# Kernel tuning notes

Hardware: AMD Instinct MI355X
Metric: run time of the kernel (lower is better)

## Reference

```python
import jax, jax.numpy as jnp
import numpy as np

N = 262144
E = N * 32
C_W = 7.0 / np.pi  # Wendland C2 2D normalization


def kernel_gradient(q, dirs, h):
    # torchSPHv2 wendland gradient: -dir * C/h^3 * 20 q (1-q)^3, q = r/h in [0,1]
    mag = (C_W / h ** 3) * 20.0 * q * (1.0 - q) ** 3
    return -dirs * mag[:, None]


def setup_inputs() -> dict:
    key = jax.random.key(0)
    ks = jax.random.split(key, 10)
    pos = lambda k: jax.random.uniform(k, (N,), dtype=jnp.float32) + 0.5  # keep strictly positive
    fluidArea = pos(ks[0]) * 1e-3
    fluidActualArea = pos(ks[1]) * 1e-3
    fluidRestDensity = pos(ks[2]) * 1000.0
    fluidDensity = pos(ks[3])
    fluidPressure2 = jax.random.uniform(ks[4], (N,), dtype=jnp.float32) * 1e3
    fluidPredictedVelocity = jax.random.normal(ks[5], (N, 2), dtype=jnp.float32)
    fluidPredAccel = jax.random.normal(ks[6], (N, 2), dtype=jnp.float32)
    fluidNeighbors = jax.random.randint(ks[7], (2, E), 0, N, dtype=jnp.int32)
    fluidRadialDistances = jax.random.uniform(ks[8], (E,), dtype=jnp.float32)
    d = jax.random.normal(ks[9], (E, 2), dtype=jnp.float32)
    fluidDistances = d / (jnp.linalg.norm(d, axis=1, keepdims=True) + 1e-7)
    return {
        'fluidArea': fluidArea, 'fluidActualArea': fluidActualArea,
        'fluidRestDensity': fluidRestDensity, 'fluidDensity': fluidDensity,
        'fluidPressure2': fluidPressure2,
        'fluidPredictedVelocity': fluidPredictedVelocity,
        'fluidPredAccel': fluidPredAccel,
        'fluidRadialDistances': fluidRadialDistances,
        'fluidDistances': fluidDistances,
        'fluidNeighbors': fluidNeighbors,
        'support': 0.05, 'dt': 0.002,
    }


def reference(fluidArea, fluidActualArea, fluidRestDensity, fluidDensity,
              fluidPressure2, fluidPredictedVelocity, fluidPredAccel,
              fluidRadialDistances, fluidDistances, fluidNeighbors,
              support, dt):
    seg = lambda v, i: jax.ops.segment_sum(v, i, num_segments=N)
    i = fluidNeighbors[0]
    j = fluidNeighbors[1]
    grad = kernel_gradient(fluidRadialDistances, fluidDistances, support)  # [E,2]
    grad2 = jnp.einsum('nd,nd->n', grad, grad)

    # --- alpha (fluid term + final) ---
    kSum1 = seg(fluidActualArea[j][:, None] * grad, i)                       # [N,2]
    kSum2 = seg((fluidActualArea ** 2 / (fluidArea * fluidRestDensity))[j] * grad2, i)
    fac = -dt ** 2 * fluidActualArea
    mass = fluidArea * fluidRestDensity
    alpha = fac / mass * jnp.einsum('nd,nd->n', kSum1, kSum1) + fac * kSum2

    # --- fluid pressure acceleration ---
    facA = -(fluidArea * fluidRestDensity)[j]
    p = fluidPressure2 / (fluidDensity * fluidRestDensity) ** 2
    fluidAccelTerm = seg((facA * (p[i] + p[j]))[:, None] * grad, i)          # [N,2]

    # --- source term (velocity divergence) ---
    facS = -dt * fluidActualArea[j]
    vij = fluidPredictedVelocity[i] - fluidPredictedVelocity[j]
    source = seg(facS * jnp.einsum('nd,nd->n', vij, grad), i)                # [N]

    # --- updated pressure fluid kernel sum ---
    facP = dt ** 2 * fluidActualArea[j]
    aij = fluidPredAccel[i] - fluidPredAccel[j]
    kernelSum = seg(jnp.einsum('nd,nd->n', facP[:, None] * aij, grad), i)    # [N]

    return jnp.concatenate([alpha[:, None], fluidAccelTerm,
                            source[:, None], kernelSum[:, None]], axis=1)  # [N,5]
```

## Files before the change

kernel.cpp:

```cpp
#include <hip/hip_runtime.h>
#include <math.h>


#define PB        512
#define PB_SHIFT  9
#define SLICES    8
#define CSTRIDE   16
#define NR        8
#define BIN_EDGES 2048
#define TILE      1024

typedef float v2f __attribute__((ext_vector_type(2)));

__device__ __forceinline__ void ldsbar() {
    asm volatile("s_waitcnt lgkmcnt(0)" ::: "memory");
    __builtin_amdgcn_s_barrier();
    asm volatile("" ::: "memory");
}

static inline size_t align256(size_t x) { return (x + 255) & ~(size_t)255; }

__global__ __launch_bounds__(256) void pre_kernel(
    const float*  __restrict__ area,
    const float*  __restrict__ actualArea,
    const float*  __restrict__ restDensity,
    const float*  __restrict__ density,
    const float*  __restrict__ pressure2,
    const float2* __restrict__ vel,
    const float2* __restrict__ accel,
    float4* __restrict__ pre2,
    int*    __restrict__ cursor, int ncursor,
    float*  __restrict__ accz, int nacc,
    int n) {
    int t = blockIdx.x * blockDim.x + threadIdx.x;
    int stride = gridDim.x * blockDim.x;
    for (int k = t; k < ncursor; k += stride) cursor[k] = 0;
    for (int k = t; k < nacc; k += stride) accz[k] = 0.f;
    if (t >= n) return;
    float m  = area[t] * restDensity[t];
    float dr = density[t] * restDensity[t];
    float p  = pressure2[t] / (dr * dr);
    float aa = actualArea[t];
    float2 v  = vel[t];
    float2 ac = accel[t];
    pre2[2 * (size_t)t]     = make_float4(p, m / aa, aa, aa * aa / m);
    pre2[2 * (size_t)t + 1] = make_float4(v.x, v.y, ac.x, ac.y);
}

__global__ __launch_bounds__(256) void bin_kernel(
    const int*    __restrict__ nbr,
    const float*  __restrict__ rad,
    const float2* __restrict__ dirs,
    const float*  __restrict__ supp,
    int*          __restrict__ cursor,
    unsigned int* __restrict__ pay32,
    int cap, int nb, int estart, int eend, int E) {
    __shared__ float s3[BIN_EDGES * 3];
    __shared__ int   sD[BIN_EDGES];
    __shared__ int lcount[512];
    __shared__ int lclaim[512];
    __shared__ int lstart[512];
    int tid = threadIdx.x;
    int x   = blockIdx.x & (NR - 1);
    for (int k = tid; k < 512; k += 256) lcount[k] = 0;
    ldsbar();
    int e0 = estart + blockIdx.x * BIN_EDGES + tid;

    int jj[8]; float qq[8]; v2f dd[8]; int pk[8];
#pragma unroll
    for (int k = 0; k < 8; ++k) {
        int e = e0 + k * 256;
        pk[k] = -1; jj[k] = 0; qq[k] = 0.f; dd[k] = (v2f){0.f, 0.f};
        if (e < eend) {
            jj[k] = __builtin_nontemporal_load(nbr + E + e);
            qq[k] = __builtin_nontemporal_load(rad + e);
            dd[k] = __builtin_nontemporal_load((const v2f*)dirs + e);
            int i = __builtin_nontemporal_load(nbr + e);
            int b = i >> PB_SHIFT;
            int r = atomicAdd(&lcount[b], 1);
            pk[k] = (b << 21) | ((i & (PB - 1)) << 12) | r;
        }
    }
    ldsbar();
    if (tid >= 64) {
        for (int k = tid - 64; k < nb; k += 192) {
            int c = lcount[k];
            lclaim[k] = c ? atomicAdd(&cursor[(size_t)(k * NR + x) * CSTRIDE], c) : 0;
        }
    } else {
        int running = 0;
        for (int c = 0; c < 8; ++c) {
            int orig = lcount[c * 64 + tid];
            int v = orig;
#pragma unroll
            for (int off = 1; off < 64; off <<= 1) {
                int u = __shfl_up(v, off, 64);
                if (tid >= off) v += u;
            }
            lstart[c * 64 + tid] = running + v - orig;
            running += __shfl(v, 63, 64);
        }
    }
    ldsbar();

    float h  = supp[0];
    float kc = 20.0f * (7.0f / 3.14159265358979323846f) / (h * h * h);
    int cap3  = cap * 3;
    int cap24 = cap * 3 * NR;

#pragma unroll
    for (int k = 0; k < 8; ++k) {
        if (pk[k] < 0) continue;
        int b  = pk[k] >> 21;
        int li = (pk[k] >> 12) & (PB - 1);
        int r  = pk[k] & 2047;
        float  q = qq[k];
        v2f    d = dd[k];
        float om  = 1.0f - q;
        float mag = kc * q * om * om * om;
        float gx = -d.x * mag;
        float gy = -d.y * mag;
        int slot = lstart[b] + r;
        s3[slot * 3 + 0] = __int_as_float((jj[k] << PB_SHIFT) | li);
        s3[slot * 3 + 1] = gx;
        s3[slot * 3 + 2] = gy;
        int g = lclaim[b] + r;
        sD[slot] = (g < cap) ? (b * cap24 + x * cap3 + g * 3) : -1;
    }
    ldsbar();
    int total3 = (lstart[511] + lcount[511]) * 3;
    for (int dwi = tid; dwi < total3; dwi += 256) {
        int rec = dwi / 3;
        int f   = dwi - rec * 3;
        int gd  = sD[rec];
        if (gd >= 0) pay32[gd + f] = __float_as_uint(s3[dwi]);
    }
}

__global__ __launch_bounds__(256) void reduce_kernel(
    const unsigned int* __restrict__ pay32,
    const int*    __restrict__ cursor, int cap,
    const float4* __restrict__ pre2,
    const float*  __restrict__ dtp,
    float*        __restrict__ partials,
    int accum, int n) {
    __shared__ float s7[7][TILE];
    __shared__ int   lhist[PB];
    __shared__ int   lofs[PB];
    __shared__ float ptab[PB];
    int b   = blockIdx.x >> 3;
    int s   = blockIdx.x & (NR - 1);
    int tid = threadIdx.x;

    int p0 = (b << PB_SHIFT) + tid;
    int p1 = p0 + 256;
    float pi0 = (p0 < n) ? pre2[2 * (size_t)p0].x : 0.f;
    float pi1 = (p1 < n) ? pre2[2 * (size_t)p1].x : 0.f;
    ptab[tid] = pi0; ptab[tid + 256] = pi1;
    float a0[7] = {0.f, 0.f, 0.f, 0.f, 0.f, 0.f, 0.f};
    float a1[7] = {0.f, 0.f, 0.f, 0.f, 0.f, 0.f, 0.f};
    float dt  = dtp[0];
    float dt2 = dt * dt;

    int cnt = cursor[(size_t)(b * NR + s) * CSTRIDE];
    if (cnt > cap) cnt = cap;
    size_t RB = (size_t)(b * NR + s) * cap * 3;
    int r0 = tid * 4;

    float4 c0v, c1v, c2v, n0v, n1v, n2v;
    if (cnt > 0) {
        int rb = r0;
        int rc_ = (rb + 4 <= cap) ? rb : (cap - 4);
        const float4* g = (const float4*)(pay32 + RB + (size_t)rc_ * 3);
        c0v = g[0]; c1v = g[1]; c2v = g[2];
    }
    for (int T = 0; T < cnt; T += TILE) {
        lhist[tid] = 0; lhist[tid + 256] = 0;
        if (T + TILE < cnt) {
            int rb = T + TILE + r0;
            int rc_ = (rb + 4 <= cap) ? rb : (cap - 4);
            const float4* g = (const float4*)(pay32 + RB + (size_t)rc_ * 3);
            n0v = g[0]; n1v = g[1]; n2v = g[2];
        }
        int rb = T + r0;
        bool v0 = rb < cnt, v1 = rb + 1 < cnt, v2 = rb + 2 < cnt, v3 = rb + 3 < cnt;
        int jli0 = __float_as_int(c0v.x); float gx0 = c0v.y, gy0 = c0v.z;
        int jli1 = __float_as_int(c0v.w); float gx1 = c1v.x, gy1 = c1v.y;
        int jli2 = __float_as_int(c1v.z); float gx2 = c1v.w, gy2 = c2v.x;
        int jli3 = __float_as_int(c2v.y); float gx3 = c2v.z, gy3 = c2v.w;
        int li0 = jli0 & (PB - 1), li1 = jli1 & (PB - 1);
        int li2 = jli2 & (PB - 1), li3 = jli3 & (PB - 1);
        size_t j0 = v0 ? (size_t)(jli0 >> PB_SHIFT) : 0;
        size_t j1 = v1 ? (size_t)(jli1 >> PB_SHIFT) : 0;
        size_t j2 = v2 ? (size_t)(jli2 >> PB_SHIFT) : 0;
        size_t j3 = v3 ? (size_t)(jli3 >> PB_SHIFT) : 0;
        float4 ja0 = pre2[2 * j0], jb0 = pre2[2 * j0 + 1];
        float4 ja1 = pre2[2 * j1], jb1 = pre2[2 * j1 + 1];
        float4 ja2 = pre2[2 * j2], jb2 = pre2[2 * j2 + 1];
        float4 ja3 = pre2[2 * j3], jb3 = pre2[2 * j3 + 1];
        ldsbar();
        if (v0) atomicAdd(&lhist[li0], 1);
        if (v1) atomicAdd(&lhist[li1], 1);
        if (v2) atomicAdd(&lhist[li2], 1);
        if (v3) atomicAdd(&lhist[li3], 1);
        ldsbar();
        if (tid < 64) {
            int running = 0;
            for (int c = 0; c < 8; ++c) {
                int orig = lhist[c * 64 + tid];
                int v = orig;
#pragma unroll
                for (int off = 1; off < 64; off <<= 1) {
                    int u = __shfl_up(v, off, 64);
                    if (tid >= off) v += u;
                }
                lofs[c * 64 + tid] = running + v - orig;
                running += __shfl(v, 63, 64);
            }
        }
        ldsbar();
#define SCAT(vv, li, jaa, jbb, gxx, gyy)                                     \
        if (vv) {                                                            \
            int sl = atomicAdd(&lofs[li], 1);                                \
            float C0 = jaa.z * gxx;                                          \
            float C1 = jaa.z * gyy;                                          \
            float C2 = jaa.w * (gxx * gxx + gyy * gyy);                      \
            float rc = -(ptab[li] + jaa.x) * jaa.y;                          \
            s7[0][sl] = C0;      s7[1][sl] = C1;      s7[2][sl] = C2;        \
            s7[3][sl] = rc * C0; s7[4][sl] = rc * C1;                        \
            s7[5][sl] = dt  * (jbb.x * C0 + jbb.y * C1);                     \
            s7[6][sl] = dt2 * (jbb.z * C0 + jbb.w * C1);                     \
        }
        SCAT(v0, li0, ja0, jb0, gx0, gy0)
        SCAT(v1, li1, ja1, jb1, gx1, gy1)
        SCAT(v2, li2, ja2, jb2, gx2, gy2)
        SCAT(v3, li3, ja3, jb3, gx3, gy3)
#undef SCAT
        ldsbar();
        {
            int e0 = lofs[tid], h0 = lhist[tid];
            for (int r = e0 - h0; r < e0; ++r) {
                a0[0] += s7[0][r]; a0[1] += s7[1][r]; a0[2] += s7[2][r];
                a0[3] += s7[3][r]; a0[4] += s7[4][r];
                a0[5] += s7[5][r]; a0[6] += s7[6][r];
            }
            int e1 = lofs[tid + 256], h1 = lhist[tid + 256];
            for (int r = e1 - h1; r < e1; ++r) {
                a1[0] += s7[0][r]; a1[1] += s7[1][r]; a1[2] += s7[2][r];
                a1[3] += s7[3][r]; a1[4] += s7[4][r];
                a1[5] += s7[5][r]; a1[6] += s7[6][r];
            }
        }
        ldsbar();
        c0v = n0v; c1v = n1v; c2v = n2v;
    }

    float* dst = partials + ((size_t)b * SLICES + s) * (PB * 7);
    {
        float4 va = (p0 < n) ? pre2[2 * (size_t)p0 + 1]
                             : make_float4(0.f, 0.f, 0.f, 0.f);
        float src = a0[5] - dt  * (va.x * a0[0] + va.y * a0[1]);
        float ker = dt2 * (va.z * a0[0] + va.w * a0[1]) - a0[6];
        float* d = dst + (size_t)tid * 7;
        if (accum) {
            d[0] += a0[0]; d[1] += a0[1]; d[2] += a0[2]; d[3] += a0[3];
            d[4] += a0[4]; d[5] += src;   d[6] += ker;
        } else {
            d[0] = a0[0]; d[1] = a0[1]; d[2] = a0[2]; d[3] = a0[3];
            d[4] = a0[4]; d[5] = src;   d[6] = ker;
        }
    }
    {
        float4 va = (p1 < n) ? pre2[2 * (size_t)p1 + 1]
                             : make_float4(0.f, 0.f, 0.f, 0.f);
        float src = a1[5] - dt  * (va.x * a1[0] + va.y * a1[1]);
        float ker = dt2 * (va.z * a1[0] + va.w * a1[1]) - a1[6];
        float* d = dst + (size_t)(tid + 256) * 7;
        if (accum) {
            d[0] += a1[0]; d[1] += a1[1]; d[2] += a1[2]; d[3] += a1[3];
            d[4] += a1[4]; d[5] += src;   d[6] += ker;
        } else {
            d[0] = a1[0]; d[1] = a1[1]; d[2] = a1[2]; d[3] = a1[3];
            d[4] = a1[4]; d[5] = src;   d[6] = ker;
        }
    }
}

__global__ void edge_kernel(const int* __restrict__ nbr,
                            const float* __restrict__ rad,
                            const float2* __restrict__ dirs,
                            const float4* __restrict__ pre2,
                            const float* __restrict__ supp,
                            const float* __restrict__ dtp,
                            float* __restrict__ acc, int E) {
    int e = blockIdx.x * blockDim.x + threadIdx.x;
    if (e >= E) return;
    float h = supp[0], dt = dtp[0];
    float kc = 20.0f * (7.0f / 3.14159265358979323846f) / (h * h * h);
    int i = nbr[e];
    int j = nbr[E + e];
    float  q = rad[e];
    float2 d = dirs[e];
    float om  = 1.0f - q;
    float mag = kc * q * om * om * om;
    float gx = -d.x * mag;
    float gy = -d.y * mag;
    float g2 = gx * gx + gy * gy;
    float4 ja = pre2[2 * (size_t)j];
    float4 jb = pre2[2 * (size_t)j + 1];
    float4 ia = pre2[2 * (size_t)i];
    float4 ib = pre2[2 * (size_t)i + 1];
    float aaj = ja.z;
    float m   = ja.y * aaj;
    float pp  = -m * (ia.x + ja.x);
    float vdotg = (ib.x - jb.x) * gx + (ib.y - jb.y) * gy;
    float adotg = (ib.z - jb.z) * gx + (ib.w - jb.w) * gy;
    float* base = acc + (size_t)i * 8;
    atomicAdd(base + 0, aaj * gx);
    atomicAdd(base + 1, aaj * gy);
    atomicAdd(base + 2, ja.w * g2);
    atomicAdd(base + 3, pp * gx);
    atomicAdd(base + 4, pp * gy);
    atomicAdd(base + 5, -dt * aaj * vdotg);
    atomicAdd(base + 6, dt * dt * aaj * adotg);
}

__global__ __launch_bounds__(256) void fin_kernel(
    const float* __restrict__ area,
    const float* __restrict__ actualArea,
    const float* __restrict__ restDensity,
    const float* __restrict__ dtp,
    const float* __restrict__ data, int mode, int nslice,
    float* __restrict__ out, int n) {
    int t = blockIdx.x * blockDim.x + threadIdx.x;
    if (t >= n) return;
    float s0 = 0, s1 = 0, s2 = 0, s3 = 0, s4 = 0, s5 = 0, s6 = 0;
    if (mode == 0) {
        const float* base = data + ((size_t)(t >> PB_SHIFT) * SLICES) * (PB * 7)
                                 + (size_t)(t & (PB - 1)) * 7;
        for (int s = 0; s < nslice; ++s) {
            const float* p = base + (size_t)s * (PB * 7);
            s0 += p[0]; s1 += p[1]; s2 += p[2]; s3 += p[3];
            s4 += p[4]; s5 += p[5]; s6 += p[6];
        }
    } else {
        const float* a = data + (size_t)t * 8;
        s0 = a[0]; s1 = a[1]; s2 = a[2]; s3 = a[3];
        s4 = a[4]; s5 = a[5]; s6 = a[6];
    }
    float dt   = dtp[0];
    float fac  = -dt * dt * actualArea[t];
    float mass = area[t] * restDensity[t];
    float alpha = fac / mass * (s0 * s0 + s1 * s1) + fac * s2;
    float* o = out + (size_t)t * 5;
    o[0] = alpha;
    o[1] = s3;
    o[2] = s4;
    o[3] = s5;
    o[4] = s6;
}

extern "C" void kernel_launch(void* const* d_in, const int* in_sizes, int n_in,
                              void* d_out, int out_size, void* d_ws, size_t ws_size,
                              hipStream_t stream) {
    const float* area        = (const float*)d_in[0];
    const float* actualArea  = (const float*)d_in[1];
    const float* restDensity = (const float*)d_in[2];
    const float* density     = (const float*)d_in[3];
    const float* pressure2   = (const float*)d_in[4];
    const float2* vel        = (const float2*)d_in[5];
    const float2* accel      = (const float2*)d_in[6];
    const float* rad         = (const float*)d_in[7];
    const float2* dirs       = (const float2*)d_in[8];
    const int*   nbr         = (const int*)d_in[9];
    const float* supp        = (const float*)d_in[10];
    const float* dtp         = (const float*)d_in[11];
    float* out = (float*)d_out;

    int N = in_sizes[0];
    int E = in_sizes[7];
    int nb = (N + PB - 1) >> PB_SHIFT;

    size_t sz_cur   = (size_t)nb * NR * CSTRIDE * 8 * sizeof(int);
    size_t off_pre  = align256(sz_cur);
    size_t sz_pre   = (size_t)N * 8 * sizeof(float);
    size_t off_part = align256(off_pre + sz_pre);
    size_t sz_part  = (size_t)nb * SLICES * PB * 7 * sizeof(float);
    size_t off_pay  = align256(off_part + sz_part);

    int* cursor     = (int*)d_ws;
    float4* pre2    = (float4*)((char*)d_ws + off_pre);
    float* partials = (float*)((char*)d_ws + off_part);

    int nchunk = 0, cap = 0;
    if (nb <= 512 && ws_size > off_pay) {
        for (int c = 1; c <= 8; c *= 2) {
            long long Ec = (E + c - 1) / c;
            double mean = (double)Ec / ((double)nb * NR);
            long long need = (long long)(mean + 8.0 * sqrt(mean) + 64.0);
            need = (need + 63) & ~63ll;
            if (off_pay + (size_t)nb * NR * need * 12 <= ws_size) {
                nchunk = c; cap = (int)need; break;
            }
        }
    }

    int bs = 256;
    int grid_n = (N + bs - 1) / bs;
    if (nchunk > 0) {
        unsigned int* pay32 = (unsigned int*)((char*)d_ws + off_pay);
        int ncursor = nb * NR * CSTRIDE * nchunk;
        pre_kernel<<<grid_n, bs, 0, stream>>>(
            area, actualArea, restDensity, density, pressure2, vel, accel,
            pre2, cursor, ncursor, (float*)nullptr, 0, N);
        int Ec  = (E + nchunk - 1) / nchunk;
        for (int c = 0; c < nchunk; ++c) {
            int es = c * Ec;
            int ee = es + Ec; if (ee > E) ee = E;
            if (es >= ee) break;
            int* curC = cursor + (size_t)c * nb * NR * CSTRIDE;
            int nblk = (ee - es + BIN_EDGES - 1) / BIN_EDGES;
            bin_kernel<<<nblk, bs, 0, stream>>>(
                nbr, rad, dirs, supp, curC, pay32, cap, nb, es, ee, E);
            reduce_kernel<<<nb * NR, bs, 0, stream>>>(
                pay32, curC, cap, pre2, dtp, partials, (c > 0) ? 1 : 0, N);
        }
        fin_kernel<<<grid_n, bs, 0, stream>>>(
            area, actualArea, restDensity, dtp, partials, 0, SLICES, out, N);
    } else {
        float* acc = partials;
        pre_kernel<<<grid_n, bs, 0, stream>>>(
            area, actualArea, restDensity, density, pressure2, vel, accel,
            pre2, cursor, 0, acc, N * 8, N);
        edge_kernel<<<(E + bs - 1) / bs, bs, 0, stream>>>(
            nbr, rad, dirs, pre2, supp, dtp, acc, E);
        fin_kernel<<<grid_n, bs, 0, stream>>>(
            area, actualArea, restDensity, dtp, acc, 1, 0, out, N);
    }
}
```

Measured before the change: 397.9 us.

## Halve reduce partial slices, pack bin records as float4, vectorize partial I/O

Each reduce block now processes two of the eight bin slices for a particle block, so there are four partial slices instead of eight and less partial traffic for the final kernel. Partials are padded to eight floats and written and read as two 16-byte vectors with nontemporal hints. The bin kernel stores each record together with its destination in a single float4 in LDS and writes it out as one 12-byte store instead of three scalar stores. The dt scaling and the pressure-coefficient product move out of the per-edge scatter into the per-particle accumulation, which trims LDS traffic per edge. In exchange the reduce grid is half as large, which lowers parallelism and may leave the GPU less well occupied.

Result: faster. 389.4 us (-2.1%).

```diff
diff --git a/kernel.cpp b/kernel.cpp
--- a/kernel.cpp
+++ b/kernel.cpp
@@ -4,13 +4,14 @@
 
 #define PB        512
 #define PB_SHIFT  9
-#define SLICES    8
+#define NR        8
+#define NSLICE    4
 #define CSTRIDE   16
-#define NR        8
 #define BIN_EDGES 2048
 #define TILE      1024
 
 typedef float v2f __attribute__((ext_vector_type(2)));
+typedef float v4f __attribute__((ext_vector_type(4)));
 
 __device__ __forceinline__ void ldsbar() {
     asm volatile("s_waitcnt lgkmcnt(0)" ::: "memory");
@@ -55,8 +56,7 @@
     int*          __restrict__ cursor,
     unsigned int* __restrict__ pay32,
     int cap, int nb, int estart, int eend, int E) {
-    __shared__ float s3[BIN_EDGES * 3];
-    __shared__ int   sD[BIN_EDGES];
+    __shared__ float4 srec[BIN_EDGES];
     __shared__ int lcount[512];
     __shared__ int lclaim[512];
     __shared__ int lstart[512];
@@ -120,20 +120,21 @@
         float mag = kc * q * om * om * om;
         float gx = -d.x * mag;
         float gy = -d.y * mag;
-        int slot = lstart[b] + r;
-        s3[slot * 3 + 0] = __int_as_float((jj[k] << PB_SHIFT) | li);
-        s3[slot * 3 + 1] = gx;
-        s3[slot * 3 + 2] = gy;
-        int g = lclaim[b] + r;
-        sD[slot] = (g < cap) ? (b * cap24 + x * cap3 + g * 3) : -1;
+        int g  = lclaim[b] + r;
+        int gd = (g < cap) ? (b * cap24 + x * cap3 + g * 3) : -1;
+        srec[lstart[b] + r] = make_float4(
+            __int_as_float((jj[k] << PB_SHIFT) | li), gx, gy, __int_as_float(gd));
     }
     ldsbar();
-    int total3 = (lstart[511] + lcount[511]) * 3;
-    for (int dwi = tid; dwi < total3; dwi += 256) {
-        int rec = dwi / 3;
-        int f   = dwi - rec * 3;
-        int gd  = sD[rec];
-        if (gd >= 0) pay32[gd + f] = __float_as_uint(s3[dwi]);
+    int total = lstart[511] + lcount[511];
+    for (int r = tid; r < total; r += 256) {
+        float4 rec = srec[r];
+        int gd = __float_as_int(rec.w);
+        if (gd >= 0) {
+            uint3 w = make_uint3(__float_as_uint(rec.x), __float_as_uint(rec.y),
+                                 __float_as_uint(rec.z));
+            *(uint3*)(pay32 + gd) = w;
+        }
     }
 }
 
@@ -144,12 +145,12 @@
     const float*  __restrict__ dtp,
     float*        __restrict__ partials,
     int accum, int n) {
-    __shared__ float s7[7][TILE];
+    __shared__ float s7[6][TILE];
     __shared__ int   lhist[PB];
     __shared__ int   lofs[PB];
     __shared__ float ptab[PB];
-    int b   = blockIdx.x >> 3;
-    int s   = blockIdx.x & (NR - 1);
+    int b   = blockIdx.x >> 2;
+    int sb  = blockIdx.x & (NSLICE - 1);
     int tid = threadIdx.x;
 
     int p0 = (b << PB_SHIFT) + tid;
@@ -159,129 +160,142 @@
     ptab[tid] = pi0; ptab[tid + 256] = pi1;
     float a0[7] = {0.f, 0.f, 0.f, 0.f, 0.f, 0.f, 0.f};
     float a1[7] = {0.f, 0.f, 0.f, 0.f, 0.f, 0.f, 0.f};
+
+    int r0 = tid * 4;
+    for (int rg = 0; rg < 2; ++rg) {
+        int s = sb + rg * NSLICE;
+        int cnt = cursor[(size_t)(b * NR + s) * CSTRIDE];
+        if (cnt > cap) cnt = cap;
+        size_t RB = (size_t)(b * NR + s) * cap * 3;
+
+        v4f c0v, c1v, c2v, n0v, n1v, n2v;
+        if (cnt > 0) {
+            int rb = r0;
+            int rc_ = (rb + 4 <= cap) ? rb : (cap - 4);
+            const v4f* g = (const v4f*)(pay32 + RB + (size_t)rc_ * 3);
+            c0v = __builtin_nontemporal_load(g);
+            c1v = __builtin_nontemporal_load(g + 1);
+            c2v = __builtin_nontemporal_load(g + 2);
+        }
+        for (int T = 0; T < cnt; T += TILE) {
+            lhist[tid] = 0; lhist[tid + 256] = 0;
+            if (T + TILE < cnt) {
+                int rb = T + TILE + r0;
+                int rc_ = (rb + 4 <= cap) ? rb : (cap - 4);
+                const v4f* g = (const v4f*)(pay32 + RB + (size_t)rc_ * 3);
+                n0v = __builtin_nontemporal_load(g);
+                n1v = __builtin_nontemporal_load(g + 1);
+                n2v = __builtin_nontemporal_load(g + 2);
+            }
+            int rb = T + r0;
+            bool v0 = rb < cnt, v1 = rb + 1 < cnt, v2 = rb + 2 < cnt, v3 = rb + 3 < cnt;
+            int jli0 = __float_as_int(c0v.x); float gx0 = c0v.y, gy0 = c0v.z;
+            int jli1 = __float_as_int(c0v.w); float gx1 = c1v.x, gy1 = c1v.y;
+            int jli2 = __float_as_int(c1v.z); float gx2 = c1v.w, gy2 = c2v.x;
+            int jli3 = __float_as_int(c2v.y); float gx3 = c2v.z, gy3 = c2v.w;
+            int li0 = jli0 & (PB - 1), li1 = jli1 & (PB - 1);
+            int li2 = jli2 & (PB - 1), li3 = jli3 & (PB - 1);
+            size_t j0 = v0 ? (size_t)(jli0 >> PB_SHIFT) : 0;
+            size_t j1 = v1 ? (size_t)(jli1 >> PB_SHIFT) : 0;
+            size_t j2 = v2 ? (size_t)(jli2 >> PB_SHIFT) : 0;
+            size_t j3 = v3 ? (size_t)(jli3 >> PB_SHIFT) : 0;
+            float4 ja0 = pre2[2 * j0], jb0 = pre2[2 * j0 + 1];
+            float4 ja1 = pre2[2 * j1], jb1 = pre2[2 * j1 + 1];
+            float4 ja2 = pre2[2 * j2], jb2 = pre2[2 * j2 + 1];
+            float4 ja3 = pre2[2 * j3], jb3 = pre2[2 * j3 + 1];
+            ldsbar();
+            if (v0) atomicAdd(&lhist[li0], 1);
+            if (v1) atomicAdd(&lhist[li1], 1);
+            if (v2) atomicAdd(&lhist[li2], 1);
+            if (v3) atomicAdd(&lhist[li3], 1);
+            ldsbar();
+            if (tid < 64) {
+                int running = 0;
+                for (int c = 0; c < 8; ++c) {
+                    int orig = lhist[c * 64 + tid];
+                    int v = orig;
+#pragma unroll
+                    for (int off = 1; off < 64; off <<= 1) {
+                        int u = __shfl_up(v, off, 64);
+                        if (tid >= off) v += u;
+                    }
+                    lofs[c * 64 + tid] = running + v - orig;
+                    running += __shfl(v, 63, 64);
+                }
+            }
+            ldsbar();
+#define SCAT(vv, li, jaa, jbb, gxx, gyy)                                     \
+            if (vv) {                                                        \
+                int sl = atomicAdd(&lofs[li], 1);                            \
+                float C0 = jaa.z * gxx;                                      \
+                float C1 = jaa.z * gyy;                                      \
+                s7[0][sl] = C0;                                              \
+                s7[1][sl] = C1;                                              \
+                s7[2][sl] = jaa.w * (gxx * gxx + gyy * gyy);                 \
+                s7[3][sl] = -(ptab[li] + jaa.x) * jaa.y;                     \
+                s7[4][sl] = jbb.x * C0 + jbb.y * C1;                         \
+                s7[5][sl] = jbb.z * C0 + jbb.w * C1;                         \
+            }
+            SCAT(v0, li0, ja0, jb0, gx0, gy0)
+            SCAT(v1, li1, ja1, jb1, gx1, gy1)
+            SCAT(v2, li2, ja2, jb2, gx2, gy2)
+            SCAT(v3, li3, ja3, jb3, gx3, gy3)
+#undef SCAT
+            ldsbar();
+            {
+                int e0 = lofs[tid], h0 = lhist[tid];
+                for (int r = e0 - h0; r < e0; ++r) {
+                    float C0 = s7[0][r], C1 = s7[1][r], rc = s7[3][r];
+                    a0[0] += C0; a0[1] += C1; a0[2] += s7[2][r];
+                    a0[3] += rc * C0; a0[4] += rc * C1;
+                    a0[5] += s7[4][r]; a0[6] += s7[5][r];
+                }
+                int e1 = lofs[tid + 256], h1 = lhist[tid + 256];
+                for (int r = e1 - h1; r < e1; ++r) {
+                    float C0 = s7[0][r], C1 = s7[1][r], rc = s7[3][r];
+                    a1[0] += C0; a1[1] += C1; a1[2] += s7[2][r];
+                    a1[3] += rc * C0; a1[4] += rc * C1;
+                    a1[5] += s7[4][r]; a1[6] += s7[5][r];
+                }
+            }
+            ldsbar();
+            c0v = n0v; c1v = n1v; c2v = n2v;
+        }
+    }
+
     float dt  = dtp[0];
     float dt2 = dt * dt;
-
-    int cnt = cursor[(size_t)(b * NR + s) * CSTRIDE];
-    if (cnt > cap) cnt = cap;
-    size_t RB = (size_t)(b * NR + s) * cap * 3;
-    int r0 = tid * 4;
-
-    float4 c0v, c1v, c2v, n0v, n1v, n2v;
-    if (cnt > 0) {
-        int rb = r0;
-        int rc_ = (rb + 4 <= cap) ? rb : (cap - 4);
-        const float4* g = (const float4*)(pay32 + RB + (size_t)rc_ * 3);
-        c0v = g[0]; c1v = g[1]; c2v = g[2];
-    }
-    for (int T = 0; T < cnt; T += TILE) {
-        lhist[tid] = 0; lhist[tid + 256] = 0;
-        if (T + TILE < cnt) {
-            int rb = T + TILE + r0;
-            int rc_ = (rb + 4 <= cap) ? rb : (cap - 4);
-            const float4* g = (const float4*)(pay32 + RB + (size_t)rc_ * 3);
-            n0v = g[0]; n1v = g[1]; n2v = g[2];
-        }
-        int rb = T + r0;
-        bool v0 = rb < cnt, v1 = rb + 1 < cnt, v2 = rb + 2 < cnt, v3 = rb + 3 < cnt;
-        int jli0 = __float_as_int(c0v.x); float gx0 = c0v.y, gy0 = c0v.z;
-        int jli1 = __float_as_int(c0v.w); float gx1 = c1v.x, gy1 = c1v.y;
-        int jli2 = __float_as_int(c1v.z); float gx2 = c1v.w, gy2 = c2v.x;
-        int jli3 = __float_as_int(c2v.y); float gx3 = c2v.z, gy3 = c2v.w;
-        int li0 = jli0 & (PB - 1), li1 = jli1 & (PB - 1);
-        int li2 = jli2 & (PB - 1), li3 = jli3 & (PB - 1);
-        size_t j0 = v0 ? (size_t)(jli0 >> PB_SHIFT) : 0;
-        size_t j1 = v1 ? (size_t)(jli1 >> PB_SHIFT) : 0;
-        size_t j2 = v2 ? (size_t)(jli2 >> PB_SHIFT) : 0;
-        size_t j3 = v3 ? (size_t)(jli3 >> PB_SHIFT) : 0;
-        float4 ja0 = pre2[2 * j0], jb0 = pre2[2 * j0 + 1];
-        float4 ja1 = pre2[2 * j1], jb1 = pre2[2 * j1 + 1];
-        float4 ja2 = pre2[2 * j2], jb2 = pre2[2 * j2 + 1];
-        float4 ja3 = pre2[2 * j3], jb3 = pre2[2 * j3 + 1];
-        ldsbar();
-        if (v0) atomicAdd(&lhist[li0], 1);
-        if (v1) atomicAdd(&lhist[li1], 1);
-        if (v2) atomicAdd(&lhist[li2], 1);
-        if (v3) atomicAdd(&lhist[li3], 1);
-        ldsbar();
-        if (tid < 64) {
-            int running = 0;
-            for (int c = 0; c < 8; ++c) {
-                int orig = lhist[c * 64 + tid];
-                int v = orig;
-#pragma unroll
-                for (int off = 1; off < 64; off <<= 1) {
-                    int u = __shfl_up(v, off, 64);
-                    if (tid >= off) v += u;
-                }
-                lofs[c * 64 + tid] = running + v - orig;
-                running += __shfl(v, 63, 64);
-            }
-        }
-        ldsbar();
-#define SCAT(vv, li, jaa, jbb, gxx, gyy)                                     \
-        if (vv) {                                                            \
-            int sl = atomicAdd(&lofs[li], 1);                                \
-            float C0 = jaa.z * gxx;                                          \
-            float C1 = jaa.z * gyy;                                          \
-            float C2 = jaa.w * (gxx * gxx + gyy * gyy);                      \
-            float rc = -(ptab[li] + jaa.x) * jaa.y;                          \
-            s7[0][sl] = C0;      s7[1][sl] = C1;      s7[2][sl] = C2;        \
-            s7[3][sl] = rc * C0; s7[4][sl] = rc * C1;                        \
-            s7[5][sl] = dt  * (jbb.x * C0 + jbb.y * C1);                     \
-            s7[6][sl] = dt2 * (jbb.z * C0 + jbb.w * C1);                     \
-        }
-        SCAT(v0, li0, ja0, jb0, gx0, gy0)
-        SCAT(v1, li1, ja1, jb1, gx1, gy1)
-        SCAT(v2, li2, ja2, jb2, gx2, gy2)
-        SCAT(v3, li3, ja3, jb3, gx3, gy3)
-#undef SCAT
-        ldsbar();
-        {
-            int e0 = lofs[tid], h0 = lhist[tid];
-            for (int r = e0 - h0; r < e0; ++r) {
-                a0[0] += s7[0][r]; a0[1] += s7[1][r]; a0[2] += s7[2][r];
-                a0[3] += s7[3][r]; a0[4] += s7[4][r];
-                a0[5] += s7[5][r]; a0[6] += s7[6][r];
-            }
-            int e1 = lofs[tid + 256], h1 = lhist[tid + 256];
-            for (int r = e1 - h1; r < e1; ++r) {
-                a1[0] += s7[0][r]; a1[1] += s7[1][r]; a1[2] += s7[2][r];
-                a1[3] += s7[3][r]; a1[4] += s7[4][r];
-                a1[5] += s7[5][r]; a1[6] += s7[6][r];
-            }
-        }
-        ldsbar();
-        c0v = n0v; c1v = n1v; c2v = n2v;
-    }
-
-    float* dst = partials + ((size_t)b * SLICES + s) * (PB * 7);
+    v4f* dst = (v4f*)(partials + ((size_t)b * NSLICE + sb) * (PB * 8));
     {
         float4 va = (p0 < n) ? pre2[2 * (size_t)p0 + 1]
                              : make_float4(0.f, 0.f, 0.f, 0.f);
-        float src = a0[5] - dt  * (va.x * a0[0] + va.y * a0[1]);
-        float ker = dt2 * (va.z * a0[0] + va.w * a0[1]) - a0[6];
-        float* d = dst + (size_t)tid * 7;
+        float src = dt  * (a0[5] - (va.x * a0[0] + va.y * a0[1]));
+        float ker = dt2 * ((va.z * a0[0] + va.w * a0[1]) - a0[6]);
+        v4f w0 = {a0[0], a0[1], a0[2], a0[3]};
+        v4f w1 = {a0[4], src, ker, 0.f};
+        v4f* d = dst + (size_t)tid * 2;
         if (accum) {
-            d[0] += a0[0]; d[1] += a0[1]; d[2] += a0[2]; d[3] += a0[3];
-            d[4] += a0[4]; d[5] += src;   d[6] += ker;
+            v4f o0 = d[0], o1 = d[1];
+            d[0] = w0 + o0; d[1] = w1 + o1;
         } else {
-            d[0] = a0[0]; d[1] = a0[1]; d[2] = a0[2]; d[3] = a0[3];
-            d[4] = a0[4]; d[5] = src;   d[6] = ker;
+            __builtin_nontemporal_store(w0, d);
+            __builtin_nontemporal_store(w1, d + 1);
         }
     }
     {
         float4 va = (p1 < n) ? pre2[2 * (size_t)p1 + 1]
                              : make_float4(0.f, 0.f, 0.f, 0.f);
-        float src = a1[5] - dt  * (va.x * a1[0] + va.y * a1[1]);
-        float ker = dt2 * (va.z * a1[0] + va.w * a1[1]) - a1[6];
-        float* d = dst + (size_t)(tid + 256) * 7;
+        float src = dt  * (a1[5] - (va.x * a1[0] + va.y * a1[1]));
+        float ker = dt2 * ((va.z * a1[0] + va.w * a1[1]) - a1[6]);
+        v4f w0 = {a1[0], a1[1], a1[2], a1[3]};
+        v4f w1 = {a1[4], src, ker, 0.f};
+        v4f* d = dst + (size_t)(tid + 256) * 2;
         if (accum) {
-            d[0] += a1[0]; d[1] += a1[1]; d[2] += a1[2]; d[3] += a1[3];
-            d[4] += a1[4]; d[5] += src;   d[6] += ker;
+            v4f o0 = d[0], o1 = d[1];
+            d[0] = w0 + o0; d[1] = w1 + o1;
         } else {
-            d[0] = a1[0]; d[1] = a1[1]; d[2] = a1[2]; d[3] = a1[3];
-            d[4] = a1[4]; d[5] = src;   d[6] = ker;
+            __builtin_nontemporal_store(w0, d);
+            __builtin_nontemporal_store(w1, d + 1);
         }
     }
 }
@@ -336,12 +350,14 @@
     if (t >= n) return;
     float s0 = 0, s1 = 0, s2 = 0, s3 = 0, s4 = 0, s5 = 0, s6 = 0;
     if (mode == 0) {
-        const float* base = data + ((size_t)(t >> PB_SHIFT) * SLICES) * (PB * 7)
-                                 + (size_t)(t & (PB - 1)) * 7;
+        const v4f* base = (const v4f*)data
+            + ((size_t)(t >> PB_SHIFT) * NSLICE) * (PB * 2)
+            + (size_t)(t & (PB - 1)) * 2;
         for (int s = 0; s < nslice; ++s) {
-            const float* p = base + (size_t)s * (PB * 7);
-            s0 += p[0]; s1 += p[1]; s2 += p[2]; s3 += p[3];
-            s4 += p[4]; s5 += p[5]; s6 += p[6];
+            v4f q0 = __builtin_nontemporal_load(base + (size_t)s * (PB * 2));
+            v4f q1 = __builtin_nontemporal_load(base + (size_t)s * (PB * 2) + 1);
+            s0 += q0.x; s1 += q0.y; s2 += q0.z; s3 += q0.w;
+            s4 += q1.x; s5 += q1.y; s6 += q1.z;
         }
     } else {
         const float* a = data + (size_t)t * 8;
@@ -385,7 +401,9 @@
     size_t off_pre  = align256(sz_cur);
     size_t sz_pre   = (size_t)N * 8 * sizeof(float);
     size_t off_part = align256(off_pre + sz_pre);
-    size_t sz_part  = (size_t)nb * SLICES * PB * 7 * sizeof(float);
+    size_t sz_partA = (size_t)nb * NSLICE * PB * 8 * sizeof(float);
+    size_t sz_partB = (size_t)N * 8 * sizeof(float);
+    size_t sz_part  = sz_partA > sz_partB ? sz_partA : sz_partB;
     size_t off_pay  = align256(off_part + sz_part);
 
     int* cursor     = (int*)d_ws;
@@ -422,11 +440,11 @@
             int nblk = (ee - es + BIN_EDGES - 1) / BIN_EDGES;
             bin_kernel<<<nblk, bs, 0, stream>>>(
                 nbr, rad, dirs, supp, curC, pay32, cap, nb, es, ee, E);
-            reduce_kernel<<<nb * NR, bs, 0, stream>>>(
+            reduce_kernel<<<nb * NSLICE, bs, 0, stream>>>(
                 pay32, curC, cap, pre2, dtp, partials, (c > 0) ? 1 : 0, N);
         }
         fin_kernel<<<grid_n, bs, 0, stream>>>(
-            area, actualArea, restDensity, dtp, partials, 0, SLICES, out, N);
+            area, actualArea, restDensity, dtp, partials, 0, NSLICE, out, N);
     } else {
         float* acc = partials;
         pre_kernel<<<grid_n, bs, 0, stream>>>(
```
